# Kernel tuning notes

Measured on AMD Instinct MI355X. Metric: run time of the kernel, lower is better.

Reference implementation:

```python
import jax, jax.numpy as jnp
import numpy as np

MODEL_DIM = 1024
HEAD_DIM = 64
BATCH = 4
SEQ = 4096


def setup_inputs() -> dict:
    key = jax.random.key(0)
    ks = jax.random.split(key, 7)
    s = 1.0 / np.sqrt(MODEL_DIM)
    x = jax.random.normal(ks[0], (BATCH, SEQ, MODEL_DIM), dtype=jnp.float32)
    # causal lower-triangular boolean mask, broadcast over batch
    mask = jnp.tril(jnp.ones((SEQ, SEQ), dtype=jnp.bool_))
    Wk = jax.random.uniform(ks[1], (MODEL_DIM, HEAD_DIM), jnp.float32, -s, s)
    bk = jax.random.uniform(ks[2], (HEAD_DIM,), jnp.float32, -s, s)
    Wq = jax.random.uniform(ks[3], (MODEL_DIM, HEAD_DIM), jnp.float32, -s, s)
    bq = jax.random.uniform(ks[4], (HEAD_DIM,), jnp.float32, -s, s)
    Wv = jax.random.uniform(ks[5], (MODEL_DIM, HEAD_DIM), jnp.float32, -s, s)
    bv = jax.random.uniform(ks[6], (HEAD_DIM,), jnp.float32, -s, s)
    return {"x": x, "mask": mask, "Wk": Wk, "bk": bk, "Wq": Wq, "bq": bq, "Wv": Wv, "bv": bv}


def reference(x, mask, Wk, bk, Wq, bq, Wv, bv):
    # K, Q, V: (B, S, Dh)
    K = jnp.einsum('bsd,dh->bsh', x, Wk) + bk
    Q = jnp.einsum('bsd,dh->bsh', x, Wq) + bq
    V = jnp.einsum('bsd,dh->bsh', x, Wv) + bv
    scale = 1.0 / jnp.sqrt(jnp.asarray(HEAD_DIM, dtype=x.dtype))
    G = jnp.einsum('bqh,bkh->bqk', Q, K) * scale  # (B, S, S)
    G = jnp.where(mask[None, :, :], G, -jnp.inf)
    G = jax.nn.softmax(G, axis=-1)
    # dropout is identity at inference (eval mode)
    attn = jnp.einsum('bqk,bkh->bqh', G, V)
    return attn
```

## Files before the change

### kernel.cpp

```cpp
#include <hip/hip_runtime.h>
#include <hip/hip_bf16.h>
#include <stdint.h>

typedef __attribute__((ext_vector_type(8))) short bf16x8;
typedef __attribute__((ext_vector_type(4))) short bf16x4;
typedef __attribute__((ext_vector_type(4))) float f32x4;
typedef __attribute__((ext_vector_type(4))) unsigned short us4;

#define MFMA32(a, b, c) __builtin_amdgcn_mfma_f32_16x16x32_bf16(a, b, c, 0, 0, 0)

#if defined(__has_builtin) && __has_builtin(__builtin_amdgcn_mfma_f32_16x16x16bf16_1k)
__device__ __forceinline__ f32x4 MFMA16(bf16x4 a, bf16x4 b, f32x4 c) {
    return __builtin_amdgcn_mfma_f32_16x16x16bf16_1k(a, b, c, 0, 0, 0);
}
#elif defined(__has_builtin) && __has_builtin(__builtin_amdgcn_mfma_f32_16x16x16_bf16)
__device__ __forceinline__ f32x4 MFMA16(bf16x4 a, bf16x4 b, f32x4 c) {
    return __builtin_amdgcn_mfma_f32_16x16x16_bf16(a, b, c, 0, 0, 0);
}
#else
__device__ __forceinline__ f32x4 MFMA16(bf16x4 a, bf16x4 b, f32x4 c) {
    f32x4 d;
    asm volatile("v_mfma_f32_16x16x16_bf16 %0, %1, %2, %3\n\ts_nop 7\n\ts_nop 2"
                 : "=v"(d) : "v"(a), "v"(b), "v"(c));
    return d;
}
#endif

__device__ __forceinline__ short f2bf(float f) {
    union { float f; uint32_t u; } v; v.f = f;
    uint32_t u = v.u;
    u = (u + 0x7FFFu + ((u >> 16) & 1u)) >> 16;
    return (short)u;
}
__device__ __forceinline__ float bf2f(short s) {
    union { uint32_t u; float f; } v; v.u = ((uint32_t)(unsigned short)s) << 16;
    return v.f;
}
__device__ __forceinline__ uint32_t cvt_pk_bf16(float lo, float hi) {
    uint32_t r;
    asm("v_cvt_pk_bf16_f32 %0, %1, %2" : "=v"(r) : "v"(lo), "v"(hi));
    return r;
}

#define QSCALE 0.18033688011112042f

__global__ void wt_prep(const float* __restrict__ Wk, const float* __restrict__ bk,
                        const float* __restrict__ Wq, const float* __restrict__ bq,
                        const float* __restrict__ Wv, const float* __restrict__ bv,
                        short* __restrict__ WT, float* __restrict__ biasC) {
    int i = blockIdx.x * 256 + threadIdx.x;
    if (i < 192 * 1024) {
        int c = i >> 10, k = i & 1023, cc = c & 63;
        const float* W; float sc;
        if (c < 64)       { W = Wq; sc = QSCALE; }
        else if (c < 128) { W = Wk; sc = 1.0f;   }
        else              { W = Wv; sc = 1.0f;   }
        WT[i] = f2bf(W[k * 64 + cc] * sc);
    }
    if (blockIdx.x == 0 && threadIdx.x < 192) {
        int c = threadIdx.x;
        float bb;
        if (c < 64)       bb = bq[c] * QSCALE;
        else if (c < 128) bb = bk[c - 64];
        else              bb = bv[c - 128];
        biasC[c] = bb;
    }
}

__global__ __launch_bounds__(256) void qkv_proj(
        const float* __restrict__ X, const short* __restrict__ WT,
        const float* __restrict__ biasC,
        short* __restrict__ Qb, short* __restrict__ Kb, short* __restrict__ Vt) {
    union SM {
        short stage[16][1032];
        float merge[12][16][4][17];
    };
    __shared__ SM sm;
    const int t = threadIdx.x;
    const int lane = t & 63, w = t >> 6, l15 = lane & 15, h = lane >> 4;
    const int row0 = blockIdx.x * 16;

    {
        const int srow = t >> 4, sl = t & 15;
        const float* xr = X + (size_t)(row0 + srow) * 1024 + sl * 8;
        short* dr = &sm.stage[srow][sl * 8];
#pragma unroll
        for (int it = 0; it < 8; it++) {
            const float4 a0 = *(const float4*)(xr + it * 128);
            const float4 a1 = *(const float4*)(xr + it * 128 + 4);
            uint4 pk;
            pk.x = cvt_pk_bf16(a0.x, a0.y);
            pk.y = cvt_pk_bf16(a0.z, a0.w);
            pk.z = cvt_pk_bf16(a1.x, a1.y);
            pk.w = cvt_pk_bf16(a1.z, a1.w);
            *(uint4*)(dr + it * 128) = pk;
        }
    }
    __syncthreads();

    f32x4 acc[12];
#pragma unroll
    for (int ct = 0; ct < 12; ct++) acc[ct] = (f32x4){0.f, 0.f, 0.f, 0.f};

    const short* ar = &sm.stage[l15][w * 256 + h * 8];
    const short* wb = WT + (size_t)l15 * 1024 + w * 256 + h * 8;

    for (int kc = 0; kc < 256; kc += 32) {
        const bf16x8 af = *(const bf16x8*)(ar + kc);
#pragma unroll
        for (int ct = 0; ct < 12; ct++) {
            const bf16x8 bf = *(const bf16x8*)(wb + (size_t)ct * 16 * 1024 + kc);
            acc[ct] = MFMA32(af, bf, acc[ct]);
        }
    }
    __syncthreads();

#pragma unroll
    for (int ct = 0; ct < 12; ct++)
#pragma unroll
        for (int r = 0; r < 4; r++)
            sm.merge[ct][h * 4 + r][w][l15] = acc[ct][r];
    __syncthreads();

    const int b = row0 >> 12, srow = row0 & 4095;

#pragma unroll
    for (int i = 0; i < 8; i++) {
        const int e = t + 256 * i;
        const int ct = e >> 8, row = (e >> 4) & 15, col = e & 15;
        float val = sm.merge[ct][row][0][col] + sm.merge[ct][row][1][col]
                  + sm.merge[ct][row][2][col] + sm.merge[ct][row][3][col]
                  + biasC[ct * 16 + col];
        if (ct < 4) Qb[(size_t)(row0 + row) * 64 + ct * 16 + col] = f2bf(val);
        else        Kb[(size_t)(row0 + row) * 64 + (ct - 4) * 16 + col] = f2bf(val);
    }
    {
        const int ctv = (t >> 4) & 3;
        const int col = t & 15;
        const int rg = t >> 6;
        const int hd = ctv * 16 + col;
        const float bias = biasC[128 + hd];
        us4 pk;
#pragma unroll
        for (int r = 0; r < 4; r++) {
            const int row = rg * 4 + r;
            float val = sm.merge[8 + ctv][row][0][col] + sm.merge[8 + ctv][row][1][col]
                      + sm.merge[8 + ctv][row][2][col] + sm.merge[8 + ctv][row][3][col] + bias;
            pk[r] = (unsigned short)f2bf(val);
        }
        *(us4*)(Vt + ((size_t)(b * 64 + hd)) * 4096 + srow + rg * 4) = pk;
    }
}

__device__ __forceinline__ void softmax_update(const f32x4 s[4], float& m, float& l,
                                               f32x4 o[4], bf16x4 pb[4]) {
    float mx = s[0][0];
#pragma unroll
    for (int c = 0; c < 4; c++)
#pragma unroll
        for (int r = 0; r < 4; r++) mx = fmaxf(mx, s[c][r]);
    mx = fmaxf(mx, __shfl_xor(mx, 16));
    mx = fmaxf(mx, __shfl_xor(mx, 32));
    const float mn = fmaxf(m, mx);
    const float fac = exp2f(m - mn);
    m = mn;
    float p[4][4];
    float sum = 0.f;
#pragma unroll
    for (int c = 0; c < 4; c++)
#pragma unroll
        for (int r = 0; r < 4; r++) { p[c][r] = exp2f(s[c][r] - mn); sum += p[c][r]; }
    sum += __shfl_xor(sum, 16);
    sum += __shfl_xor(sum, 32);
    l = l * fac + sum;
#pragma unroll
    for (int c = 0; c < 4; c++) o[c] *= fac;
#pragma unroll
    for (int c = 0; c < 4; c++) {
        union { bf16x4 v; uint32_t u[2]; } pk;
        pk.u[0] = cvt_pk_bf16(p[c][0], p[c][1]);
        pk.u[1] = cvt_pk_bf16(p[c][2], p[c][3]);
        pb[c] = pk.v;
    }
}

__global__ __launch_bounds__(256) void attn(
        const short* __restrict__ Qb, const short* __restrict__ Kb,
        const short* __restrict__ Vt,
        short* __restrict__ PO, float* __restrict__ PM, float* __restrict__ PL) {
    const int lane = threadIdx.x & 63, wg = threadIdx.x >> 6;
    const int l15 = lane & 15, h = lane >> 4;
    const int j = blockIdx.x;
    const int b = j / 320, jj = j - b * 320;
    int u, c;
    if (jj < 32)       { u = jj;                 c = 0; }
    else if (jj < 96)  { u = 32 + ((jj - 32) >> 1);  c = (jj - 32) & 1; }
    else if (jj < 192) { const int q3 = (jj - 96) / 3; u = 64 + q3; c = (jj - 96) - 3 * q3; }
    else               { u = 96 + ((jj - 192) >> 2); c = (jj - 192) & 3; }
    const int row32 = u * 32;
    const int lt = u >> 1;
    const int tend = min(c * 16 + 15, lt);
    const size_t bbase = (size_t)b * 4096 * 64;

    const short* qp0 = Qb + bbase + (size_t)(row32 + l15) * 64 + h * 8;
    const short* qp1 = qp0 + 16 * 64;
    const bf16x8 q00 = *(const bf16x8*)qp0,  q01 = *(const bf16x8*)(qp0 + 32);
    const bf16x8 q10 = *(const bf16x8*)qp1,  q11 = *(const bf16x8*)(qp1 + 32);

    f32x4 o0[4], o1[4];
    float m0 = -__builtin_inff(), m1 = -__builtin_inff(), l0 = 0.f, l1 = 0.f;
#pragma unroll
    for (int t = 0; t < 4; t++) { o0[t] = (f32x4){0,0,0,0}; o1[t] = (f32x4){0,0,0,0}; }

    for (int kt = c * 16 + wg; kt <= tend; kt += 4) {
        const short* kb = Kb + bbase + (size_t)kt * 64 * 64;
        f32x4 s0[4], s1[4];
#pragma unroll
        for (int cc = 0; cc < 4; cc++) {
            const short* kp = kb + (size_t)(cc * 16 + l15) * 64 + h * 8;
            const bf16x8 kf0 = *(const bf16x8*)kp;
            const bf16x8 kf1 = *(const bf16x8*)(kp + 32);
            f32x4 z = (f32x4){0,0,0,0};
            z = MFMA32(kf0, q00, z);  s0[cc] = MFMA32(kf1, q01, z);
            z = (f32x4){0,0,0,0};
            z = MFMA32(kf0, q10, z);  s1[cc] = MFMA32(kf1, q11, z);
        }
        if (kt == lt) {
            const int q0g = row32 + l15, q1g = q0g + 16;
#pragma unroll
            for (int cc = 0; cc < 4; cc++) {
#pragma unroll
                for (int r = 0; r < 4; r++) {
                    const int key = kt * 64 + cc * 16 + h * 4 + r;
                    if (key > q0g) s0[cc][r] = -1e30f;
                    if (key > q1g) s1[cc][r] = -1e30f;
                }
            }
        }
        bf16x4 pb0[4], pb1[4];
        softmax_update(s0, m0, l0, o0, pb0);
        softmax_update(s1, m1, l1, o1, pb1);

        const short* vb = Vt + (size_t)b * 64 * 4096 + kt * 64;
#pragma unroll
        for (int ct = 0; ct < 4; ct++) {
            const short* vp = vb + (size_t)(ct * 16 + l15) * 4096 + h * 4;
#pragma unroll
            for (int cc = 0; cc < 4; cc++) {
                const bf16x4 vf = *(const bf16x4*)(vp + cc * 16);
                o0[ct] = MFMA16(vf, pb0[cc], o0[ct]);
                o1[ct] = MFMA16(vf, pb1[cc], o1[ct]);
            }
        }
    }

    __shared__ float c_m[4][32], c_l[4][32];
    __shared__ short c_ob[4][32][72];
    if (h == 0) {
        c_m[wg][l15] = m0;  c_m[wg][16 + l15] = m1;
        c_l[wg][l15] = l0;  c_l[wg][16 + l15] = l1;
    }
#pragma unroll
    for (int ct = 0; ct < 4; ct++) {
        *(uint32_t*)&c_ob[wg][l15][ct * 16 + h * 4]          = cvt_pk_bf16(o0[ct][0], o0[ct][1]);
        *(uint32_t*)&c_ob[wg][l15][ct * 16 + h * 4 + 2]      = cvt_pk_bf16(o0[ct][2], o0[ct][3]);
        *(uint32_t*)&c_ob[wg][16 + l15][ct * 16 + h * 4]     = cvt_pk_bf16(o1[ct][0], o1[ct][1]);
        *(uint32_t*)&c_ob[wg][16 + l15][ct * 16 + h * 4 + 2] = cvt_pk_bf16(o1[ct][2], o1[ct][3]);
    }
    __syncthreads();

    const int e = threadIdx.x;
    const int q = e >> 3, d0 = (e & 7) * 8;
    float M = fmaxf(fmaxf(c_m[0][q], c_m[1][q]), fmaxf(c_m[2][q], c_m[3][q]));
    float L = 0.f;
    float acc[8];
#pragma unroll
    for (int i = 0; i < 8; i++) acc[i] = 0.f;
#pragma unroll
    for (int ww = 0; ww < 4; ww++) {
        const float ew = exp2f(c_m[ww][q] - M);
        L += ew * c_l[ww][q];
        const bf16x8 ov = *(const bf16x8*)&c_ob[ww][q][d0];
#pragma unroll
        for (int i = 0; i < 8; i++) acc[i] += ew * bf2f(ov[i]);
    }
    if ((e & 7) == 0) { PM[(size_t)j * 32 + q] = M; PL[(size_t)j * 32 + q] = L; }
    uint4 pk;
    pk.x = cvt_pk_bf16(acc[0], acc[1]);
    pk.y = cvt_pk_bf16(acc[2], acc[3]);
    pk.z = cvt_pk_bf16(acc[4], acc[5]);
    pk.w = cvt_pk_bf16(acc[6], acc[7]);
    *(uint4*)(PO + (size_t)j * 2048 + q * 64 + d0) = pk;
}

__global__ __launch_bounds__(256) void attn_merge(
        const short* __restrict__ PO, const float* __restrict__ PM,
        const float* __restrict__ PL, float* __restrict__ out) {
    const int bu = blockIdx.x;
    const int b = bu >> 7, u = bu & 127;
    const int off = (u < 32) ? u
                 : (u < 64) ? 32 + 2 * (u - 32)
                 : (u < 96) ? 96 + 3 * (u - 64)
                 :            192 + 4 * (u - 96);
    const int nc = (u + 32) >> 5;
    const int base = b * 320 + off;
    const int e = threadIdx.x;
    const int q = e >> 3, d0 = (e & 7) * 8;

    float M = -__builtin_inff();
    for (int c = 0; c < nc; c++) M = fmaxf(M, PM[(size_t)(base + c) * 32 + q]);
    float L = 0.f;
    float acc[8];
#pragma unroll
    for (int i = 0; i < 8; i++) acc[i] = 0.f;
    for (int c = 0; c < nc; c++) {
        const size_t slot = base + c;
        const float ew = exp2f(PM[slot * 32 + q] - M);
        L += ew * PL[slot * 32 + q];
        const bf16x8 ov = *(const bf16x8*)(PO + slot * 2048 + q * 64 + d0);
#pragma unroll
        for (int i = 0; i < 8; i++) acc[i] += ew * bf2f(ov[i]);
    }
    const float inv = 1.0f / L;
    float4 w0, w1;
    w0.x = acc[0] * inv; w0.y = acc[1] * inv; w0.z = acc[2] * inv; w0.w = acc[3] * inv;
    w1.x = acc[4] * inv; w1.y = acc[5] * inv; w1.z = acc[6] * inv; w1.w = acc[7] * inv;
    float* dst = out + (size_t)b * 4096 * 64 + (size_t)(u * 32 + q) * 64 + d0;
    *(float4*)dst = w0;
    *(float4*)(dst + 4) = w1;
}

extern "C" void kernel_launch(void* const* d_in, const int* in_sizes, int n_in,
                              void* d_out, int out_size, void* d_ws, size_t ws_size,
                              hipStream_t stream) {
    const float* x  = (const float*)d_in[0];
    const float* Wk = (const float*)d_in[2];
    const float* bk = (const float*)d_in[3];
    const float* Wq = (const float*)d_in[4];
    const float* bq = (const float*)d_in[5];
    const float* Wv = (const float*)d_in[6];
    const float* bv = (const float*)d_in[7];
    float* out = (float*)d_out;

    char* ws = (char*)d_ws;
    short* WT    = (short*)(ws);
    float* biasC = (float*)(ws + 393216);
    short* Qb    = (short*)(ws + (size_t)1  * (1 << 20));
    short* Kb    = (short*)(ws + (size_t)3  * (1 << 20));
    short* Vt    = (short*)(ws + (size_t)5  * (1 << 20));
    short* PO    = (short*)(ws + (size_t)7  * (1 << 20));
    float* PM    = (float*)(ws + (size_t)13 * (1 << 20));
    float* PL    = (float*)(ws + (size_t)14 * (1 << 20));

    wt_prep<<<768, 256, 0, stream>>>(Wk, bk, Wq, bq, Wv, bv, WT, biasC);
    qkv_proj<<<1024, 256, 0, stream>>>(x, WT, biasC, Qb, Kb, Vt);
    attn<<<1280, 256, 0, stream>>>(Qb, Kb, Vt, PO, PM, PL);
    attn_merge<<<512, 256, 0, stream>>>(PO, PM, PL, out);
}
```

Baseline: 135.0 us.

## Give each wave its own key-chunk task from a longest-first table, drop LDS merge

Attention work is now split per wave instead of per block. Each wave handles one (query-row-block, 12-key-tile chunk) task, looked up from a table built in wt_prep that orders tasks longest first. Each wave writes its own partial O/m/l directly to global memory, so the in-block LDS combine and the __syncthreads are gone. The cost is more partial results for attn_merge to read and combine, and fewer, longer waves (408 blocks), which may hurt latency hiding. The fallback MFMA asm also gains an early-clobber output constraint.

```diff
diff --git a/kernel.cpp b/kernel.cpp
--- a/kernel.cpp
+++ b/kernel.cpp
@@ -21,7 +21,7 @@
 __device__ __forceinline__ f32x4 MFMA16(bf16x4 a, bf16x4 b, f32x4 c) {
     f32x4 d;
     asm volatile("v_mfma_f32_16x16x16_bf16 %0, %1, %2, %3\n\ts_nop 7\n\ts_nop 2"
-                 : "=v"(d) : "v"(a), "v"(b), "v"(c));
+                 : "=&v"(d) : "v"(a), "v"(b), "v"(c));
     return d;
 }
 #endif
@@ -43,11 +43,16 @@
 }
 
 #define QSCALE 0.18033688011112042f
+#define CH 12
+#define NTASK 408
+#define NCH(u) ((((u) >> 1) + CH) / CH)
 
 __global__ void wt_prep(const float* __restrict__ Wk, const float* __restrict__ bk,
                         const float* __restrict__ Wq, const float* __restrict__ bq,
                         const float* __restrict__ Wv, const float* __restrict__ bv,
-                        short* __restrict__ WT, float* __restrict__ biasC) {
+                        short* __restrict__ WT, float* __restrict__ biasC,
+                        unsigned char* __restrict__ TB, unsigned char* __restrict__ TC,
+                        int* __restrict__ OFF) {
     int i = blockIdx.x * 256 + threadIdx.x;
     if (i < 192 * 1024) {
         int c = i >> 10, k = i & 1023, cc = c & 63;
@@ -64,6 +69,18 @@
         else if (c < 128) bb = bk[c - 64];
         else              bb = bv[c - 128];
         biasC[c] = bb;
+    }
+    if (blockIdx.x == 1 && threadIdx.x == 0) {
+        int cum = 0;
+        for (int u = 127; u >= 0; u--) {
+            OFF[u] = cum;
+            const int nch = NCH(u);
+            for (int c = 0; c < nch; c++) {
+                TB[cum] = (unsigned char)u;
+                TC[cum] = (unsigned char)c;
+                cum++;
+            }
+        }
     }
 }
 
@@ -186,20 +203,19 @@
 
 __global__ __launch_bounds__(256) void attn(
         const short* __restrict__ Qb, const short* __restrict__ Kb,
-        const short* __restrict__ Vt,
+        const short* __restrict__ Vt, const unsigned char* __restrict__ TB,
+        const unsigned char* __restrict__ TC,
         short* __restrict__ PO, float* __restrict__ PM, float* __restrict__ PL) {
     const int lane = threadIdx.x & 63, wg = threadIdx.x >> 6;
     const int l15 = lane & 15, h = lane >> 4;
-    const int j = blockIdx.x;
-    const int b = j / 320, jj = j - b * 320;
-    int u, c;
-    if (jj < 32)       { u = jj;                 c = 0; }
-    else if (jj < 96)  { u = 32 + ((jj - 32) >> 1);  c = (jj - 32) & 1; }
-    else if (jj < 192) { const int q3 = (jj - 96) / 3; u = 64 + q3; c = (jj - 96) - 3 * q3; }
-    else               { u = 96 + ((jj - 192) >> 2); c = (jj - 192) & 3; }
+    const int gid = blockIdx.x * 4 + wg;
+    const int b = gid / NTASK, jj = gid - b * NTASK;
+    const int u = TB[jj];
+    const int c = TC[jj];
     const int row32 = u * 32;
     const int lt = u >> 1;
-    const int tend = min(c * 16 + 15, lt);
+    const int t0 = c * CH;
+    const int t1 = min(t0 + CH - 1, lt);
     const size_t bbase = (size_t)b * 4096 * 64;
 
     const short* qp0 = Qb + bbase + (size_t)(row32 + l15) * 64 + h * 8;
@@ -212,8 +228,8 @@
 #pragma unroll
     for (int t = 0; t < 4; t++) { o0[t] = (f32x4){0,0,0,0}; o1[t] = (f32x4){0,0,0,0}; }
 
-    for (int kt = c * 16 + wg; kt <= tend; kt += 4) {
-        const short* kb = Kb + bbase + (size_t)kt * 64 * 64;
+    for (int kt = t0; kt <= t1; ++kt) {
+        const short* kb = Kb + bbase + (size_t)kt * 4096;
         f32x4 s0[4], s1[4];
 #pragma unroll
         for (int cc = 0; cc < 4; cc++) {
@@ -254,56 +270,31 @@
         }
     }
 
-    __shared__ float c_m[4][32], c_l[4][32];
-    __shared__ short c_ob[4][32][72];
     if (h == 0) {
-        c_m[wg][l15] = m0;  c_m[wg][16 + l15] = m1;
-        c_l[wg][l15] = l0;  c_l[wg][16 + l15] = l1;
-    }
+        PM[(size_t)gid * 32 + l15] = m0;  PM[(size_t)gid * 32 + 16 + l15] = m1;
+        PL[(size_t)gid * 32 + l15] = l0;  PL[(size_t)gid * 32 + 16 + l15] = l1;
+    }
+    short* po = PO + (size_t)gid * 2048;
 #pragma unroll
     for (int ct = 0; ct < 4; ct++) {
-        *(uint32_t*)&c_ob[wg][l15][ct * 16 + h * 4]          = cvt_pk_bf16(o0[ct][0], o0[ct][1]);
-        *(uint32_t*)&c_ob[wg][l15][ct * 16 + h * 4 + 2]      = cvt_pk_bf16(o0[ct][2], o0[ct][3]);
-        *(uint32_t*)&c_ob[wg][16 + l15][ct * 16 + h * 4]     = cvt_pk_bf16(o1[ct][0], o1[ct][1]);
-        *(uint32_t*)&c_ob[wg][16 + l15][ct * 16 + h * 4 + 2] = cvt_pk_bf16(o1[ct][2], o1[ct][3]);
-    }
-    __syncthreads();
-
-    const int e = threadIdx.x;
-    const int q = e >> 3, d0 = (e & 7) * 8;
-    float M = fmaxf(fmaxf(c_m[0][q], c_m[1][q]), fmaxf(c_m[2][q], c_m[3][q]));
-    float L = 0.f;
-    float acc[8];
-#pragma unroll
-    for (int i = 0; i < 8; i++) acc[i] = 0.f;
-#pragma unroll
-    for (int ww = 0; ww < 4; ww++) {
-        const float ew = exp2f(c_m[ww][q] - M);
-        L += ew * c_l[ww][q];
-        const bf16x8 ov = *(const bf16x8*)&c_ob[ww][q][d0];
-#pragma unroll
-        for (int i = 0; i < 8; i++) acc[i] += ew * bf2f(ov[i]);
-    }
-    if ((e & 7) == 0) { PM[(size_t)j * 32 + q] = M; PL[(size_t)j * 32 + q] = L; }
-    uint4 pk;
-    pk.x = cvt_pk_bf16(acc[0], acc[1]);
-    pk.y = cvt_pk_bf16(acc[2], acc[3]);
-    pk.z = cvt_pk_bf16(acc[4], acc[5]);
-    pk.w = cvt_pk_bf16(acc[6], acc[7]);
-    *(uint4*)(PO + (size_t)j * 2048 + q * 64 + d0) = pk;
+        uint2 w0, w1;
+        w0.x = cvt_pk_bf16(o0[ct][0], o0[ct][1]);
+        w0.y = cvt_pk_bf16(o0[ct][2], o0[ct][3]);
+        w1.x = cvt_pk_bf16(o1[ct][0], o1[ct][1]);
+        w1.y = cvt_pk_bf16(o1[ct][2], o1[ct][3]);
+        *(uint2*)(po + (size_t)l15 * 64 + ct * 16 + h * 4) = w0;
+        *(uint2*)(po + (size_t)(16 + l15) * 64 + ct * 16 + h * 4) = w1;
+    }
 }
 
 __global__ __launch_bounds__(256) void attn_merge(
         const short* __restrict__ PO, const float* __restrict__ PM,
-        const float* __restrict__ PL, float* __restrict__ out) {
+        const float* __restrict__ PL, const int* __restrict__ OFF,
+        float* __restrict__ out) {
     const int bu = blockIdx.x;
     const int b = bu >> 7, u = bu & 127;
-    const int off = (u < 32) ? u
-                 : (u < 64) ? 32 + 2 * (u - 32)
-                 : (u < 96) ? 96 + 3 * (u - 64)
-                 :            192 + 4 * (u - 96);
-    const int nc = (u + 32) >> 5;
-    const int base = b * 320 + off;
+    const int nc = NCH(u);
+    const int base = b * NTASK + OFF[u];
     const int e = threadIdx.x;
     const int q = e >> 3, d0 = (e & 7) * 8;
 
@@ -345,15 +336,18 @@
     char* ws = (char*)d_ws;
     short* WT    = (short*)(ws);
     float* biasC = (float*)(ws + 393216);
-    short* Qb    = (short*)(ws + (size_t)1  * (1 << 20));
-    short* Kb    = (short*)(ws + (size_t)3  * (1 << 20));
-    short* Vt    = (short*)(ws + (size_t)5  * (1 << 20));
-    short* PO    = (short*)(ws + (size_t)7  * (1 << 20));
-    float* PM    = (float*)(ws + (size_t)13 * (1 << 20));
-    float* PL    = (float*)(ws + (size_t)14 * (1 << 20));
-
-    wt_prep<<<768, 256, 0, stream>>>(Wk, bk, Wq, bq, Wv, bv, WT, biasC);
+    unsigned char* TB = (unsigned char*)(ws + 394240);
+    unsigned char* TC = (unsigned char*)(ws + 395264);
+    int* OFF     = (int*)(ws + 396288);
+    short* Qb    = (short*)(ws + (size_t)1 * (1 << 20));
+    short* Kb    = (short*)(ws + (size_t)3 * (1 << 20));
+    short* Vt    = (short*)(ws + (size_t)5 * (1 << 20));
+    short* PO    = (short*)(ws + (size_t)7 * (1 << 20));
+    float* PM    = (float*)(ws + 14024704);
+    float* PL    = (float*)(ws + 14233600);
+
+    wt_prep<<<768, 256, 0, stream>>>(Wk, bk, Wq, bq, Wv, bv, WT, biasC, TB, TC, OFF);
     qkv_proj<<<1024, 256, 0, stream>>>(x, WT, biasC, Qb, Kb, Vt);
-    attn<<<1280, 256, 0, stream>>>(Qb, Kb, Vt, PO, PM, PL);
-    attn_merge<<<512, 256, 0, stream>>>(PO, PM, PL, out);
-}
+    attn<<<408, 256, 0, stream>>>(Qb, Kb, Vt, TB, TC, PO, PM, PL);
+    attn_merge<<<512, 256, 0, stream>>>(PO, PM, PL, OFF, out);
+}
```

Measured after the change: 158.8 us. 17.7% more time.
